# Performance work log

Measured on AMD Instinct MI355X. Metric: run time of the kernel, lower is better.

The kernel has to match this reference:

```python
import jax, jax.numpy as jnp
import numpy as np

DIM = 1024
DEPTH = 6
HEADS = 16
FF = 4 * DIM
EPS = 1e-5


def _layernorm(x, g, b):
    mu = jnp.mean(x, axis=-1, keepdims=True)
    var = jnp.mean(jnp.square(x - mu), axis=-1, keepdims=True)
    return (x - mu) * jax.lax.rsqrt(var + EPS) * g + b


def setup_inputs() -> dict:
    key = jax.random.key(0)
    ks = jax.random.split(key, 16)
    s = 0.02
    inp = {
        "x": jax.random.normal(ks[0], (2, 1024, DIM), dtype=jnp.float32),
        "relative_position_bias": jax.random.normal(ks[1], (1, HEADS, 1024, 1024), dtype=jnp.float32),
        # stacked per-layer params [DEPTH, ...]
        "ln1_g": jnp.ones((DEPTH, DIM), jnp.float32),
        "ln1_b": jnp.zeros((DEPTH, DIM), jnp.float32),
        "w_qkv": jax.random.normal(ks[2], (DEPTH, DIM, 3 * DIM), dtype=jnp.float32) * s,
        "w_out": jax.random.normal(ks[3], (DEPTH, DIM, DIM), dtype=jnp.float32) * s,
        "b_out": jnp.zeros((DEPTH, DIM), jnp.float32),
        "ln2_g": jnp.ones((DEPTH, DIM), jnp.float32),
        "ln2_b": jnp.zeros((DEPTH, DIM), jnp.float32),
        "w1": jax.random.normal(ks[4], (DEPTH, DIM, FF), dtype=jnp.float32) * s,
        "b1": jnp.zeros((DEPTH, FF), jnp.float32),
        "w2": jax.random.normal(ks[5], (DEPTH, FF, DIM), dtype=jnp.float32) * s,
        "b2": jnp.zeros((DEPTH, DIM), jnp.float32),
    }
    return inp


def _forward(x, relative_position_bias, ln1_g, ln1_b, w_qkv, w_out, b_out,
             ln2_g, ln2_b, w1, b1, w2, b2):
    b, n, d = x.shape
    dh = d // HEADS
    scale = dh ** -0.5
    for l in range(DEPTH):
        # attention block (pre-norm)
        h = _layernorm(x, ln1_g[l], ln1_b[l])
        qkv = h @ w_qkv[l]                                    # [b, n, 3d]
        q, k, v = jnp.split(qkv, 3, axis=-1)
        q = q.reshape(b, n, HEADS, dh).transpose(0, 2, 1, 3)  # [b, h, n, dh]
        k = k.reshape(b, n, HEADS, dh).transpose(0, 2, 1, 3)
        v = v.reshape(b, n, HEADS, dh).transpose(0, 2, 1, 3)
        scores = jnp.einsum('bhid,bhjd->bhij', q, k) * scale + relative_position_bias
        attn = jax.nn.softmax(scores, axis=-1)
        o = jnp.einsum('bhij,bhjd->bhid', attn, v)
        o = o.transpose(0, 2, 1, 3).reshape(b, n, d)
        x = x + (o @ w_out[l] + b_out[l])
        # FFN block (pre-norm)
        h = _layernorm(x, ln2_g[l], ln2_b[l])
        h = jax.nn.gelu(h @ w1[l] + b1[l], approximate=False)
        x = x + (h @ w2[l] + b2[l])
    return x


def reference(x, relative_position_bias, ln1_g, ln1_b, w_qkv, w_out, b_out,
              ln2_g, ln2_b, w1, b1, w2, b2):
    return _forward(x, relative_position_bias, ln1_g, ln1_b, w_qkv, w_out, b_out,
                    ln2_g, ln2_b, w1, b1, w2, b2)
```

## Files before the change

kernel.cpp:

```cpp
#include <hip/hip_runtime.h>
#include <stdint.h>

#define DIM   1024
#define DEPTH 6
#define HEADS 16
#define FF    4096
#define SEQ   1024
#define BATCH 2
#define ROWS  (BATCH*SEQ)
#define DH    64

typedef __bf16 bf16x8 __attribute__((ext_vector_type(8)));
typedef float  f32x4  __attribute__((ext_vector_type(4)));

__device__ __forceinline__ unsigned short f2bf(float f) {
  unsigned int u = __builtin_bit_cast(unsigned int, f);
  u += 0x7fff + ((u >> 16) & 1);
  return (unsigned short)(u >> 16);
}
__device__ __forceinline__ float bf2f(unsigned short h) {
  unsigned int u = ((unsigned int)h) << 16;
  return __builtin_bit_cast(float, u);
}

__device__ __forceinline__ void async_load16(const void* g, void* l) {
  __builtin_amdgcn_global_load_lds(
      (const __attribute__((address_space(1))) unsigned int*)g,
      (__attribute__((address_space(3))) unsigned int*)l, 16, 0, 0);
}

template<int BM, int BN, int EPI, int NBUF, int MINW>
__global__ void __launch_bounds__(256, MINW)
gemm_kernel(const unsigned short* __restrict__ A, long lda,
            const unsigned short* __restrict__ B, long ldb,
            unsigned short* __restrict__ Cb, float* __restrict__ Cf, long ldc,
            const float* __restrict__ bias1, float scale, int K)
{
  constexpr int BK = 64;
  __shared__ unsigned short As[NBUF * BM * BK];
  __shared__ unsigned short Bs[NBUF * BN * BK];

  const int tid  = threadIdx.x;
  const int row0 = blockIdx.x * BM;
  const int col0 = blockIdx.y * BN;

  constexpr int WGN = 2;
  constexpr int WGM = 2;
  constexpr int WTM = BM / WGM;
  constexpr int WTN = BN / WGN;
  constexpr int ITM = WTM / 16;
  constexpr int ITN = WTN / 16;

  const int w = tid >> 6, l = tid & 63;
  const int quad = l >> 4, r16 = l & 15;
  const int wm = (w / WGN) * WTM;
  const int wn = (w % WGN) * WTN;
  const int sw = r16 & 7;

  f32x4 acc[ITM][ITN] = {};

  constexpr int APASS = (BM * 8) / 256;
  constexpr int BPASS = (BN * 8) / 256;

  const unsigned short* Ag = A + (long)row0 * lda;
  const unsigned short* Bg = B + (long)col0 * ldb;

  auto stage = [&](int buf, long k0) {
    unsigned short* Asb = &As[buf * (BM * BK)];
    unsigned short* Bsb = &Bs[buf * (BN * BK)];
#pragma unroll
    for (int p = 0; p < APASS; p++) {
      int flat = p * 256 + tid;
      int r = flat >> 3, cl = flat & 7;
      int cg = cl ^ (r & 7);
      async_load16(Ag + (long)r * lda + k0 + cg * 8, &Asb[flat * 8]);
    }
#pragma unroll
    for (int p = 0; p < BPASS; p++) {
      int flat = p * 256 + tid;
      int r = flat >> 3, cl = flat & 7;
      int cg = cl ^ (r & 7);
      async_load16(Bg + (long)r * ldb + k0 + cg * 8, &Bsb[flat * 8]);
    }
  };

  auto compute = [&](int buf) {
    const unsigned short* Asb = &As[buf * (BM * BK)];
    const unsigned short* Bsb = &Bs[buf * (BN * BK)];
#pragma unroll
    for (int ks = 0; ks < 2; ks++) {
      const int c = ks * 4 + quad;
      bf16x8 af[ITM], bfr[ITN];
#pragma unroll
      for (int i = 0; i < ITM; i++)
        af[i] = *(const bf16x8*)&Asb[(wm + i * 16 + r16) * BK + (c ^ sw) * 8];
#pragma unroll
      for (int j = 0; j < ITN; j++)
        bfr[j] = *(const bf16x8*)&Bsb[(wn + j * 16 + r16) * BK + (c ^ sw) * 8];
#pragma unroll
      for (int i = 0; i < ITM; i++)
#pragma unroll
        for (int j = 0; j < ITN; j++)
          acc[i][j] = __builtin_amdgcn_mfma_f32_16x16x32_bf16(af[i], bfr[j], acc[i][j], 0, 0, 0);
    }
  };

  if constexpr (NBUF == 1) {
    stage(0, 0);
    __syncthreads();
    compute(0);
  } else {
    stage(0, 0);
    __syncthreads();
    int cur = 0;
    for (long k0 = BK; k0 < K; k0 += BK) {
      stage(cur ^ 1, k0);
      compute(cur);
      __syncthreads();
      cur ^= 1;
    }
    compute(cur);
  }

#pragma unroll
  for (int i = 0; i < ITM; i++) {
#pragma unroll
    for (int j = 0; j < ITN; j++) {
      const int rr = row0 + wm + i * 16 + quad * 4;
      const int cc = col0 + wn + j * 16 + r16;
#pragma unroll
      for (int r = 0; r < 4; r++) {
        const long idx = (long)(rr + r) * ldc + cc;
        float v = acc[i][j][r];
        if constexpr (EPI == 0) {
          Cb[idx] = f2bf(v);
        } else if constexpr (EPI == 2) {
          Cf[idx] += v + bias1[cc];
        } else if constexpr (EPI == 3) {
          v += bias1[cc];
          float gl = 0.5f * v * (1.0f + erff(v * 0.70710678118654752f));
          Cb[idx] = f2bf(gl);
        }
      }
    }
  }
}

__global__ void __launch_bounds__(256, 2)
k_flashattn(const unsigned short* __restrict__ qkv,
            const unsigned short* __restrict__ vT,
            const float* __restrict__ rpb,
            unsigned short* __restrict__ O)
{
  constexpr int QT = 64;
  constexpr int KT = 64;
  constexpr int NT = SEQ / KT;

  __shared__ __align__(16) unsigned short Qs[QT * DH];
  __shared__ __align__(16) unsigned short Ks[2][KT * DH];
  __shared__ __align__(16) unsigned short Vs[2][DH * KT];
  __shared__ __align__(16) unsigned short Ps[4][16 * KT];

  const int z = blockIdx.z;
  const int b_ = z >> 4, h_ = z & 15;
  const int q0 = blockIdx.x * QT;
  const int tid = threadIdx.x;
  const int w = tid >> 6, l = tid & 63;
  const int quad = l >> 4, r16 = l & 15;
  const int sw = r16 & 7;

  const unsigned short* Qg = qkv + (long)b_ * SEQ * (3 * DIM) + h_ * DH;
  const unsigned short* Kg = Qg + DIM;
  const unsigned short* Vg = vT + (long)z * DH * SEQ;
  const float* Rg = rpb + (long)h_ * SEQ * SEQ + (long)q0 * SEQ;

  auto stageKV = [&](int buf, int kt) {
#pragma unroll
    for (int p = 0; p < 2; p++) {
      int flat = p * 256 + tid;
      int r = flat >> 3, cl = flat & 7, cg = cl ^ (r & 7);
      async_load16(Kg + (long)(kt * KT + r) * (3 * DIM) + cg * 8, &Ks[buf][flat * 8]);
    }
#pragma unroll
    for (int p = 0; p < 2; p++) {
      int flat = p * 256 + tid;
      int r = flat >> 3, cl = flat & 7, cg = cl ^ (r & 7);
      async_load16(Vg + (long)r * SEQ + kt * KT + cg * 8, &Vs[buf][flat * 8]);
    }
  };

#pragma unroll
  for (int p = 0; p < 2; p++) {
    int flat = p * 256 + tid;
    int r = flat >> 3, cl = flat & 7, cg = cl ^ (r & 7);
    async_load16(Qg + (long)(q0 + r) * (3 * DIM) + cg * 8, &Qs[flat * 8]);
  }
  stageKV(0, 0);
  __syncthreads();

  bf16x8 qA[2];
#pragma unroll
  for (int ks = 0; ks < 2; ks++)
    qA[ks] = *(const bf16x8*)&Qs[(w * 16 + r16) * DH + (((ks * 4 + quad)) ^ sw) * 8];

  f32x4 Oacc[4] = {};
  float m[4], lsum[4];
#pragma unroll
  for (int r = 0; r < 4; r++) { m[r] = -1e30f; lsum[r] = 0.0f; }

  int cur = 0;
  for (int kt = 0; kt < NT; kt++) {
    if (kt + 1 < NT) stageKV(cur ^ 1, kt + 1);

    float bias[4][4];
    const float* Rt = Rg + kt * KT;
#pragma unroll
    for (int j = 0; j < 4; j++)
#pragma unroll
      for (int r = 0; r < 4; r++)
        bias[j][r] = Rt[(long)(w * 16 + quad * 4 + r) * SEQ + j * 16 + r16];

    f32x4 s[4] = {};
#pragma unroll
    for (int ks = 0; ks < 2; ks++) {
      bf16x8 kB[4];
#pragma unroll
      for (int j = 0; j < 4; j++)
        kB[j] = *(const bf16x8*)&Ks[cur][(j * 16 + r16) * DH + ((ks * 4 + quad) ^ sw) * 8];
#pragma unroll
      for (int j = 0; j < 4; j++)
        s[j] = __builtin_amdgcn_mfma_f32_16x16x32_bf16(qA[ks], kB[j], s[j], 0, 0, 0);
    }

    float sc[4][4], p_[4][4], mt[4], ts[4];
#pragma unroll
    for (int j = 0; j < 4; j++)
#pragma unroll
      for (int r = 0; r < 4; r++)
        sc[j][r] = s[j][r] * 0.125f + bias[j][r];
#pragma unroll
    for (int r = 0; r < 4; r++) {
      mt[r] = fmaxf(fmaxf(sc[0][r], sc[1][r]), fmaxf(sc[2][r], sc[3][r]));
#pragma unroll
      for (int msk = 1; msk < 16; msk <<= 1)
        mt[r] = fmaxf(mt[r], __shfl_xor(mt[r], msk));
      float mn = fmaxf(m[r], mt[r]);
      float scale = __expf(m[r] - mn);
      m[r] = mn;
#pragma unroll
      for (int j = 0; j < 4; j++) {
        p_[j][r] = __expf(sc[j][r] - mn);
        Oacc[j][r] *= scale;
      }
      ts[r] = p_[0][r] + p_[1][r] + p_[2][r] + p_[3][r];
#pragma unroll
      for (int msk = 1; msk < 16; msk <<= 1)
        ts[r] += __shfl_xor(ts[r], msk);
      lsum[r] = lsum[r] * scale + ts[r];
    }

    unsigned short* Pw = &Ps[w][0];
#pragma unroll
    for (int j = 0; j < 4; j++)
#pragma unroll
      for (int r = 0; r < 4; r++) {
        int row = quad * 4 + r;
        int col = j * 16 + r16;
        int chunk = col >> 3;
        Pw[row * KT + ((chunk ^ (row & 7)) * 8 + (col & 7))] = f2bf(p_[j][r]);
      }

#pragma unroll
    for (int ks = 0; ks < 2; ks++) {
      bf16x8 pA = *(const bf16x8*)&Pw[r16 * KT + ((ks * 4 + quad) ^ sw) * 8];
      bf16x8 vB[4];
#pragma unroll
      for (int j = 0; j < 4; j++)
        vB[j] = *(const bf16x8*)&Vs[cur][(j * 16 + r16) * KT + ((ks * 4 + quad) ^ sw) * 8];
#pragma unroll
      for (int j = 0; j < 4; j++)
        Oacc[j] = __builtin_amdgcn_mfma_f32_16x16x32_bf16(pA, vB[j], Oacc[j], 0, 0, 0);
    }

    __syncthreads();
    cur ^= 1;
  }

#pragma unroll
  for (int r = 0; r < 4; r++) {
    const float inv = 1.0f / lsum[r];
    const long rowg = (long)b_ * SEQ + q0 + w * 16 + quad * 4 + r;
#pragma unroll
    for (int j = 0; j < 4; j++)
      O[rowg * DIM + h_ * DH + j * 16 + r16] = f2bf(Oacc[j][r] * inv);
  }
}

__global__ void k_layernorm(const float* __restrict__ x, const float* __restrict__ g,
                            const float* __restrict__ b, unsigned short* __restrict__ out)
{
  const int row = blockIdx.x;
  const int t = threadIdx.x;
  float4 v = ((const float4*)(x + (long)row * DIM))[t];
  float s = v.x + v.y + v.z + v.w;
  float q = v.x * v.x + v.y * v.y + v.z * v.z + v.w * v.w;
#pragma unroll
  for (int off = 32; off > 0; off >>= 1) {
    s += __shfl_down(s, off);
    q += __shfl_down(q, off);
  }
  __shared__ float shs[4], shq[4];
  if ((t & 63) == 0) { shs[t >> 6] = s; shq[t >> 6] = q; }
  __syncthreads();
  s = shs[0] + shs[1] + shs[2] + shs[3];
  q = shq[0] + shq[1] + shq[2] + shq[3];
  const float mu  = s * (1.0f / DIM);
  const float var = q * (1.0f / DIM) - mu * mu;
  const float rs  = rsqrtf(var + 1e-5f);
  float4 gg = ((const float4*)g)[t];
  float4 bb = ((const float4*)b)[t];
  ushort4 o;
  o.x = f2bf((v.x - mu) * rs * gg.x + bb.x);
  o.y = f2bf((v.y - mu) * rs * gg.y + bb.y);
  o.z = f2bf((v.z - mu) * rs * gg.z + bb.z);
  o.w = f2bf((v.w - mu) * rs * gg.w + bb.w);
  ((ushort4*)out)[(long)row * (DIM / 4) + t] = o;
}

__global__ void k_wtrans(const float* __restrict__ w, unsigned short* __restrict__ wT,
                         int K, int N)
{
  __shared__ unsigned short tile[64][65];
  const int n0 = blockIdx.x * 64, k0 = blockIdx.y * 64;
  const int tx = threadIdx.x, ty = threadIdx.y;
#pragma unroll
  for (int i = 0; i < 16; i++)
    tile[ty + 4 * i][tx] = f2bf(w[(long)(k0 + ty + 4 * i) * N + n0 + tx]);
  __syncthreads();
#pragma unroll
  for (int i = 0; i < 16; i++)
    wT[(long)(n0 + ty + 4 * i) * K + k0 + tx] = tile[tx][ty + 4 * i];
}

__global__ void k_vtrans(const unsigned short* __restrict__ qkv, unsigned short* __restrict__ vT)
{
  __shared__ unsigned short tile[64][65];
  const int z = blockIdx.z;
  const int b_ = z >> 4, h_ = z & 15;
  const int n0 = blockIdx.x * 64;
  const int tx = threadIdx.x, ty = threadIdx.y;
  const unsigned short* src = qkv + (long)b_ * SEQ * (3 * DIM) + 2 * DIM + h_ * DH;
#pragma unroll
  for (int i = 0; i < 16; i++)
    tile[ty + 4 * i][tx] = src[(long)(n0 + ty + 4 * i) * (3 * DIM) + tx];
  __syncthreads();
  unsigned short* dst = vT + (long)z * DH * SEQ;
#pragma unroll
  for (int i = 0; i < 16; i++)
    dst[(long)(ty + 4 * i) * SEQ + n0 + tx] = tile[tx][ty + 4 * i];
}

extern "C" void kernel_launch(void* const* d_in, const int* in_sizes, int n_in,
                              void* d_out, int out_size, void* d_ws, size_t ws_size,
                              hipStream_t stream)
{
  const float* x0   = (const float*)d_in[0];
  const float* rpb  = (const float*)d_in[1];
  const float* ln1g = (const float*)d_in[2];
  const float* ln1b = (const float*)d_in[3];
  const float* wqkv = (const float*)d_in[4];
  const float* wout = (const float*)d_in[5];
  const float* bout = (const float*)d_in[6];
  const float* ln2g = (const float*)d_in[7];
  const float* ln2b = (const float*)d_in[8];
  const float* w1   = (const float*)d_in[9];
  const float* b1   = (const float*)d_in[10];
  const float* w2   = (const float*)d_in[11];
  const float* b2   = (const float*)d_in[12];
  float* x = (float*)d_out;

  char* p = (char*)d_ws;
  auto alloc = [&](size_t n) { char* r = p; p += (n + 255) & ~(size_t)255; return r; };
  unsigned short* wTqkv = (unsigned short*)alloc((size_t)3 * DIM * DIM * 2);
  unsigned short* wTout = (unsigned short*)alloc((size_t)DIM * DIM * 2);
  unsigned short* wT1   = (unsigned short*)alloc((size_t)FF * DIM * 2);
  unsigned short* wT2   = (unsigned short*)alloc((size_t)DIM * FF * 2);
  unsigned short* hbuf  = (unsigned short*)alloc((size_t)ROWS * DIM * 2);
  unsigned short* qkvb  = (unsigned short*)alloc((size_t)ROWS * 3 * DIM * 2);
  unsigned short* vTb   = (unsigned short*)alloc((size_t)BATCH * HEADS * DH * SEQ * 2);
  unsigned short* obuf  = (unsigned short*)alloc((size_t)ROWS * DIM * 2);
  unsigned short* ffnb  = (unsigned short*)alloc((size_t)ROWS * FF * 2);

  hipMemcpyAsync(x, x0, (size_t)ROWS * DIM * 4, hipMemcpyDeviceToDevice, stream);

  const dim3 tb(64, 4);
  for (int l = 0; l < DEPTH; l++) {
    const float* Wqkv = wqkv + (size_t)l * DIM * 3 * DIM;
    const float* Wout = wout + (size_t)l * DIM * DIM;
    const float* W1   = w1   + (size_t)l * DIM * FF;
    const float* W2   = w2   + (size_t)l * FF * DIM;

    k_wtrans<<<dim3(3 * DIM / 64, DIM / 64), tb, 0, stream>>>(Wqkv, wTqkv, DIM, 3 * DIM);
    k_wtrans<<<dim3(DIM / 64, DIM / 64),     tb, 0, stream>>>(Wout, wTout, DIM, DIM);
    k_wtrans<<<dim3(FF / 64, DIM / 64),      tb, 0, stream>>>(W1,   wT1,   DIM, FF);
    k_wtrans<<<dim3(DIM / 64, FF / 64),      tb, 0, stream>>>(W2,   wT2,   FF, DIM);

    k_layernorm<<<ROWS, 256, 0, stream>>>(x, ln1g + l * DIM, ln1b + l * DIM, hbuf);

    gemm_kernel<64, 128, 0, 2, 4><<<dim3(ROWS / 64, 3 * DIM / 128), 256, 0, stream>>>(
        hbuf, DIM, wTqkv, DIM, qkvb, nullptr, 3 * DIM, nullptr, 1.0f, DIM);

    k_vtrans<<<dim3(SEQ / 64, 1, BATCH * HEADS), tb, 0, stream>>>(qkvb, vTb);

    k_flashattn<<<dim3(SEQ / 64, 1, BATCH * HEADS), 256, 0, stream>>>(
        qkvb, vTb, rpb, obuf);

    gemm_kernel<64, 64, 2, 2, 4><<<dim3(ROWS / 64, DIM / 64), 256, 0, stream>>>(
        obuf, DIM, wTout, DIM, nullptr, x, DIM, bout + l * DIM, 1.0f, DIM);

    k_layernorm<<<ROWS, 256, 0, stream>>>(x, ln2g + l * DIM, ln2b + l * DIM, hbuf);

    gemm_kernel<128, 128, 3, 2, 2><<<dim3(ROWS / 128, FF / 128), 256, 0, stream>>>(
        hbuf, DIM, wT1, DIM, ffnb, nullptr, FF, b1 + l * FF, 1.0f, DIM);

    gemm_kernel<64, 64, 2, 2, 4><<<dim3(ROWS / 64, DIM / 64), 256, 0, stream>>>(
        ffnb, FF, wT2, FF, nullptr, x, DIM, b2 + l * DIM, 1.0f, FF);
  }
}
```

Before: 1.359 ms.

## Convert position bias to bf16 once, use exp2 softmax with lazy rescale

A new kernel converts the relative position bias to bf16, pre-multiplied by log2(e), once per call. The six per-layer attention passes then read half as many bias bytes. Attention now uses exp2 with a folded scale, and it rescales the running max only when the new max exceeds the old one by a threshold, which saves exp and multiply work. The four weight-transpose launches per layer are merged into one. The cost is bf16 rounding of the bias, a possible change in accuracy, and an extra conversion pass plus a 32 MB workspace buffer.

```diff
diff --git a/kernel.cpp b/kernel.cpp
--- a/kernel.cpp
+++ b/kernel.cpp
@@ -149,12 +149,14 @@
 __global__ void __launch_bounds__(256, 2)
 k_flashattn(const unsigned short* __restrict__ qkv,
             const unsigned short* __restrict__ vT,
-            const float* __restrict__ rpb,
+            const unsigned short* __restrict__ rpbh,
             unsigned short* __restrict__ O)
 {
   constexpr int QT = 64;
   constexpr int KT = 64;
   constexpr int NT = SEQ / KT;
+  constexpr float SCL2 = 0.18033688f;
+  constexpr float THR  = 11.5415603f;
 
   __shared__ __align__(16) unsigned short Qs[QT * DH];
   __shared__ __align__(16) unsigned short Ks[2][KT * DH];
@@ -172,7 +174,7 @@
   const unsigned short* Qg = qkv + (long)b_ * SEQ * (3 * DIM) + h_ * DH;
   const unsigned short* Kg = Qg + DIM;
   const unsigned short* Vg = vT + (long)z * DH * SEQ;
-  const float* Rg = rpb + (long)h_ * SEQ * SEQ + (long)q0 * SEQ;
+  const unsigned short* Rg = rpbh + (long)h_ * SEQ * SEQ + (long)q0 * SEQ;
 
   auto stageKV = [&](int buf, int kt) {
 #pragma unroll
@@ -213,12 +215,12 @@
     if (kt + 1 < NT) stageKV(cur ^ 1, kt + 1);
 
     float bias[4][4];
-    const float* Rt = Rg + kt * KT;
+    const unsigned short* Rt = Rg + kt * KT;
 #pragma unroll
     for (int j = 0; j < 4; j++)
 #pragma unroll
       for (int r = 0; r < 4; r++)
-        bias[j][r] = Rt[(long)(w * 16 + quad * 4 + r) * SEQ + j * 16 + r16];
+        bias[j][r] = bf2f(Rt[(long)(w * 16 + quad * 4 + r) * SEQ + j * 16 + r16]);
 
     f32x4 s[4] = {};
 #pragma unroll
@@ -237,26 +239,28 @@
     for (int j = 0; j < 4; j++)
 #pragma unroll
       for (int r = 0; r < 4; r++)
-        sc[j][r] = s[j][r] * 0.125f + bias[j][r];
+        sc[j][r] = __builtin_fmaf(s[j][r], SCL2, bias[j][r]);
 #pragma unroll
     for (int r = 0; r < 4; r++) {
       mt[r] = fmaxf(fmaxf(sc[0][r], sc[1][r]), fmaxf(sc[2][r], sc[3][r]));
 #pragma unroll
       for (int msk = 1; msk < 16; msk <<= 1)
         mt[r] = fmaxf(mt[r], __shfl_xor(mt[r], msk));
-      float mn = fmaxf(m[r], mt[r]);
-      float scale = __expf(m[r] - mn);
-      m[r] = mn;
-#pragma unroll
-      for (int j = 0; j < 4; j++) {
-        p_[j][r] = __expf(sc[j][r] - mn);
-        Oacc[j][r] *= scale;
+      if (mt[r] > m[r] + THR) {
+        const float rs = __builtin_amdgcn_exp2f(m[r] - mt[r]);
+        m[r] = mt[r];
+#pragma unroll
+        for (int j = 0; j < 4; j++) Oacc[j][r] *= rs;
+        lsum[r] *= rs;
       }
+#pragma unroll
+      for (int j = 0; j < 4; j++)
+        p_[j][r] = __builtin_amdgcn_exp2f(sc[j][r] - m[r]);
       ts[r] = p_[0][r] + p_[1][r] + p_[2][r] + p_[3][r];
 #pragma unroll
       for (int msk = 1; msk < 16; msk <<= 1)
         ts[r] += __shfl_xor(ts[r], msk);
-      lsum[r] = lsum[r] * scale + ts[r];
+      lsum[r] += ts[r];
     }
 
     unsigned short* Pw = &Ps[w][0];
@@ -327,11 +331,32 @@
   ((ushort4*)out)[(long)row * (DIM / 4) + t] = o;
 }
 
-__global__ void k_wtrans(const float* __restrict__ w, unsigned short* __restrict__ wT,
-                         int K, int N)
+__global__ void k_cvtrpb(const float* __restrict__ src, unsigned short* __restrict__ dst)
+{
+  const long i = ((long)blockIdx.x * 256 + threadIdx.x) * 4;
+  float4 v = *(const float4*)(src + i);
+  ushort4 o;
+  o.x = f2bf(v.x * 1.44269504f);
+  o.y = f2bf(v.y * 1.44269504f);
+  o.z = f2bf(v.z * 1.44269504f);
+  o.w = f2bf(v.w * 1.44269504f);
+  *(ushort4*)(dst + i) = o;
+}
+
+__global__ void k_wtrans_all(const float* __restrict__ wqkv, const float* __restrict__ wout,
+                             const float* __restrict__ w1,   const float* __restrict__ w2,
+                             unsigned short* __restrict__ wTqkv, unsigned short* __restrict__ wTout,
+                             unsigned short* __restrict__ wT1,   unsigned short* __restrict__ wT2)
 {
   __shared__ unsigned short tile[64][65];
-  const int n0 = blockIdx.x * 64, k0 = blockIdx.y * 64;
+  int t = blockIdx.x;
+  const float* w; unsigned short* wT; int K, N;
+  if (t < 768)        {            w = wqkv; wT = wTqkv; K = DIM; N = 3 * DIM; }
+  else if (t < 1024)  { t -= 768;  w = wout; wT = wTout; K = DIM; N = DIM; }
+  else if (t < 2048)  { t -= 1024; w = w1;   wT = wT1;   K = DIM; N = FF; }
+  else                { t -= 2048; w = w2;   wT = wT2;   K = FF;  N = DIM; }
+  const int nt = N / 64;
+  const int n0 = (t % nt) * 64, k0 = (t / nt) * 64;
   const int tx = threadIdx.x, ty = threadIdx.y;
 #pragma unroll
   for (int i = 0; i < 16; i++)
@@ -390,8 +415,11 @@
   unsigned short* vTb   = (unsigned short*)alloc((size_t)BATCH * HEADS * DH * SEQ * 2);
   unsigned short* obuf  = (unsigned short*)alloc((size_t)ROWS * DIM * 2);
   unsigned short* ffnb  = (unsigned short*)alloc((size_t)ROWS * FF * 2);
+  unsigned short* rpbh  = (unsigned short*)alloc((size_t)HEADS * SEQ * SEQ * 2);
 
   hipMemcpyAsync(x, x0, (size_t)ROWS * DIM * 4, hipMemcpyDeviceToDevice, stream);
+
+  k_cvtrpb<<<dim3(16384), 256, 0, stream>>>(rpb, rpbh);
 
   const dim3 tb(64, 4);
   for (int l = 0; l < DEPTH; l++) {
@@ -400,10 +428,8 @@
     const float* W1   = w1   + (size_t)l * DIM * FF;
     const float* W2   = w2   + (size_t)l * FF * DIM;
 
-    k_wtrans<<<dim3(3 * DIM / 64, DIM / 64), tb, 0, stream>>>(Wqkv, wTqkv, DIM, 3 * DIM);
-    k_wtrans<<<dim3(DIM / 64, DIM / 64),     tb, 0, stream>>>(Wout, wTout, DIM, DIM);
-    k_wtrans<<<dim3(FF / 64, DIM / 64),      tb, 0, stream>>>(W1,   wT1,   DIM, FF);
-    k_wtrans<<<dim3(DIM / 64, FF / 64),      tb, 0, stream>>>(W2,   wT2,   FF, DIM);
+    k_wtrans_all<<<dim3(3072), tb, 0, stream>>>(Wqkv, Wout, W1, W2,
+                                                wTqkv, wTout, wT1, wT2);
 
     k_layernorm<<<ROWS, 256, 0, stream>>>(x, ln1g + l * DIM, ln1b + l * DIM, hbuf);
 
@@ -413,7 +439,7 @@
     k_vtrans<<<dim3(SEQ / 64, 1, BATCH * HEADS), tb, 0, stream>>>(qkvb, vTb);
 
     k_flashattn<<<dim3(SEQ / 64, 1, BATCH * HEADS), 256, 0, stream>>>(
-        qkvb, vTb, rpb, obuf);
+        qkvb, vTb, rpbh, obuf);
 
     gemm_kernel<64, 64, 2, 2, 4><<<dim3(ROWS / 64, DIM / 64), 256, 0, stream>>>(
         obuf, DIM, wTout, DIM, nullptr, x, DIM, bout + l * DIM, 1.0f, DIM);
```

New measurement: 1.346 ms. No clear change (-1.0%).
